# Performance work log

Hardware: AMD Instinct MI355X
Metric: run time of the kernel (lower is better)

Reference implementation:

```python
import jax, jax.numpy as jnp
import numpy as np


def setup_inputs() -> dict:
    key = jax.random.key(0)
    k1, k2 = jax.random.split(key)
    B, N, F, K = 8, 8192, 128, 512
    x = jax.random.normal(k1, (B, N, F), dtype=jnp.float32)
    cluster_centers = jax.random.normal(k2, (K, F), dtype=jnp.float32)
    return {"x": x, "cluster_centers": cluster_centers}


def reference(x, cluster_centers):
    # same math as sqrt(sum((x - c)^2)) without the [B,N,K,F] intermediate).
    x_sq = jnp.sum(x * x, axis=-1, keepdims=True)                 # [B, N, 1]
    c_sq = jnp.sum(cluster_centers * cluster_centers, axis=-1)    # [K]
    cross = jnp.einsum("bnf,kf->bnk", x, cluster_centers)         # [B, N, K]
    d2 = jnp.maximum(x_sq + c_sq[None, None, :] - 2.0 * cross, 0.0)
    distances = jnp.sqrt(d2)                                      # [B, N, K]
    associations = jax.nn.softmax(-distances, axis=-1)            # [B, N, K]
    output = jnp.einsum("bnk,kf->bnf", associations, cluster_centers)
    return output
```

## Files before the change

kernel.cpp:

```cpp
#include <hip/hip_runtime.h>
#include <hip/hip_bf16.h>

typedef short v8s __attribute__((ext_vector_type(8)));
typedef float v16f __attribute__((ext_vector_type(16)));
typedef unsigned v2u __attribute__((ext_vector_type(2)));

#define F_ 128
#define K_ 512
#define M_ 65536
#define CB_CH 9216
#define CT_CH 8192
#define CT_BASE 73728

typedef __attribute__((address_space(1))) const char gch;
typedef __attribute__((address_space(3))) char lch;

__device__ __forceinline__ short f2bf(float f) {
    union { float f; unsigned u; } v; v.f = f;
    unsigned u = v.u;
    u = (u + 0x7FFFu + ((u >> 16) & 1u)) >> 16;
    return (short)u;
}
__device__ __forceinline__ float bf2f(short s) {
    union { float f; unsigned u; } v;
    v.u = ((unsigned)(unsigned short)s) << 16;
    return v.f;
}

#if __has_builtin(__builtin_amdgcn_permlane32_swap)
#define HAVE_PLS 1
#endif

__device__ __forceinline__ void pswap(unsigned &a, unsigned &b, int lane) {
#ifdef HAVE_PLS
    v2u r = __builtin_amdgcn_permlane32_swap(a, b, false, false);
    a = (unsigned)r.x; b = (unsigned)r.y;
#else
    unsigned sa = (unsigned)__shfl_xor((int)a, 32);
    unsigned sb = (unsigned)__shfl_xor((int)b, 32);
    if (lane & 32) a = sb; else b = sa;
#endif
}

__global__ void prep_kernel(const float* __restrict__ centers, short* __restrict__ G) {
    const int c = blockIdx.x;
    const int f = threadIdx.x;
    const int ch = c >> 6, c64 = c & 63;
    float v = centers[c * F_ + f];
    short b = f2bf(v);
    float vb = bf2f(b);
    { const int ks = f >> 4, h = (f >> 3) & 1, j = f & 7;
      G[(size_t)ch * CB_CH + (size_t)((ks * 2 + h) * 64 + c64) * 8 + j] = b; }
    { const int kap = c64 >> 4, hh = (c64 >> 3) & 1, jj = c64 & 7;
      G[CT_BASE + (size_t)ch * CT_CH + (size_t)((kap * 2 + hh) * F_ + f) * 8 + jj] = b; }
    float s = vb * vb;
    #pragma unroll
    for (int off = 1; off < 64; off <<= 1) s += __shfl_xor(s, off);
    __shared__ float part[2];
    if ((f & 63) == 0) part[f >> 6] = s;
    __syncthreads();
    if (f < 16) {
        const float csq = part[0] + part[1];
        const float chv = -0.5f * csq;
        const short vh = f2bf(chv);
        const short vl = f2bf(chv - bf2f(vh));
        const short val = (f == 0) ? vh : (f == 1) ? vl : (f == 2) ? (short)0x3F80 : (short)0;
        const int h2 = f >> 3, j2 = f & 7;
        G[(size_t)ch * CB_CH + (size_t)((16 + h2) * 64 + c64) * 8 + j2] = val;
    }
}

__global__ __launch_bounds__(512, 2) void cluster_kernel(
        const float* __restrict__ x, const short* __restrict__ G,
        float* __restrict__ out) {
    __shared__ __align__(16) short SBall[CT_BASE];
    const int tid = threadIdx.x;
    const int wave = tid >> 6, lane = tid & 63;
    const int h = lane >> 5, c32 = lane & 31;
    const int row0 = blockIdx.x * 256 + wave * 32;

    {
        lch* d = (lch*)SBall;
        #pragma unroll
        for (int t = 0; t < 18; ++t) {
            const int gbase = t * 512 + wave * 64;
            __builtin_amdgcn_global_load_lds((gch*)((const char*)G + (size_t)(gbase + lane) * 16),
                                             d + (size_t)gbase * 16, 16, 0, 0);
        }
    }

    const float4* xr4 = (const float4*)(x + (size_t)(row0 + c32) * F_);
    float4 xl[16];
    #pragma unroll
    for (int ks = 0; ks < 8; ++ks) {
        xl[2 * ks]     = xr4[ks * 4 + h * 2];
        xl[2 * ks + 1] = xr4[ks * 4 + h * 2 + 1];
    }
    v8s Bx[9];
    float xs = 0.f;
    #pragma unroll
    for (int ks = 0; ks < 8; ++ks) {
        float vv[8] = {xl[2*ks].x, xl[2*ks].y, xl[2*ks].z, xl[2*ks].w,
                       xl[2*ks+1].x, xl[2*ks+1].y, xl[2*ks+1].z, xl[2*ks+1].w};
        v8s fr;
        #pragma unroll
        for (int j = 0; j < 8; ++j) {
            short bb = f2bf(vv[j]);
            fr[j] = bb;
            float r = bf2f(bb);
            xs += r * r;
        }
        Bx[ks] = fr;
    }
    xs += __shfl_xor(xs, 32);
    {
        const float xh = -0.5f * xs;
        const short sxh = f2bf(xh);
        const short sxl = f2bf(xh - bf2f(sxh));
        v8s e = (v8s){0, 0, 0, 0, 0, 0, 0, 0};
        if (h == 0) { e[0] = (short)0x3F80; e[1] = (short)0x3F80; e[2] = sxh; e[3] = sxl; }
        Bx[8] = e;
    }

    v16f Of[4];
    #pragma unroll
    for (int ft = 0; ft < 4; ++ft)
        #pragma unroll
        for (int e2 = 0; e2 < 16; ++e2) Of[ft][e2] = 0.f;
    float lden = 0.f;

    __syncthreads();

    #pragma unroll 1
    for (int j = 0; j < 8; ++j) {
        const int ch = (wave + blockIdx.x + j) & 7;
        const short* CbS = SBall + (size_t)ch * CB_CH;
        const short* CTGc = G + CT_BASE + (size_t)ch * CT_CH;

        v8s cf0[8];
        #pragma unroll
        for (int kp = 0; kp < 2; ++kp)
            #pragma unroll
            for (int ft = 0; ft < 4; ++ft)
                cf0[kp * 4 + ft] = *(const v8s*)
                    &CTGc[(size_t)((kp * 2 + h) * F_ + ft * 32 + c32) * 8];

        v16f a0, a1;
        #pragma unroll
        for (int e2 = 0; e2 < 16; ++e2) { a0[e2] = 0.f; a1[e2] = 0.f; }
        {
            v8s f0a = *(const v8s*)&CbS[(size_t)((0 * 2 + h) * 64 + c32) * 8];
            v8s f1a = *(const v8s*)&CbS[(size_t)((0 * 2 + h) * 64 + 32 + c32) * 8];
            v8s f0b = *(const v8s*)&CbS[(size_t)((1 * 2 + h) * 64 + c32) * 8];
            v8s f1b = *(const v8s*)&CbS[(size_t)((1 * 2 + h) * 64 + 32 + c32) * 8];
            #pragma unroll
            for (int ks = 0; ks < 9; ++ks) {
                v8s c0 = f0a, c1 = f1a;
                f0a = f0b; f1a = f1b;
                if (ks < 7) {
                    f0b = *(const v8s*)&CbS[(size_t)(((ks + 2) * 2 + h) * 64 + c32) * 8];
                    f1b = *(const v8s*)&CbS[(size_t)(((ks + 2) * 2 + h) * 64 + 32 + c32) * 8];
                }
                a0 = __builtin_amdgcn_mfma_f32_32x32x16_bf16(c0, Bx[ks], a0, 0, 0, 0);
                a1 = __builtin_amdgcn_mfma_f32_32x32x16_bf16(c1, Bx[ks], a1, 0, 0, 0);
            }
        }

        unsigned U[8];
        #pragma unroll
        for (int t = 0; t < 8; ++t) {
            const float s20 = fmaxf(-4.16273796f * a0[2 * t], 0.f);
            const float s21 = fmaxf(-4.16273796f * a0[2 * t + 1], 0.f);
            const float p0 = __builtin_amdgcn_exp2f(-__builtin_amdgcn_sqrtf(s20));
            const float p1 = __builtin_amdgcn_exp2f(-__builtin_amdgcn_sqrtf(s21));
            union { __hip_bfloat162 hh; unsigned u; } cv;
            cv.hh = __float22bfloat162_rn(make_float2(p0, p1));
            U[t] = cv.u;
            lden += __uint_as_float(cv.u << 16);
            lden += __uint_as_float(cv.u & 0xffff0000u);
        }
        v8s cf1[8];
        #pragma unroll
        for (int kp = 0; kp < 2; ++kp)
            #pragma unroll
            for (int ft = 0; ft < 4; ++ft)
                cf1[kp * 4 + ft] = *(const v8s*)
                    &CTGc[(size_t)(((2 + kp) * 2 + h) * F_ + ft * 32 + c32) * 8];
        #pragma unroll
        for (int kp = 0; kp < 2; ++kp) {
            unsigned s0 = U[4 * kp],     s2 = U[4 * kp + 2];
            unsigned s1 = U[4 * kp + 1], s3 = U[4 * kp + 3];
            pswap(s0, s2, lane);
            pswap(s1, s3, lane);
            union { v8s v; unsigned u[4]; } pf;
            pf.u[0] = s0; pf.u[1] = s1; pf.u[2] = s2; pf.u[3] = s3;
            #pragma unroll
            for (int ft = 0; ft < 4; ++ft)
                Of[ft] = __builtin_amdgcn_mfma_f32_32x32x16_bf16(pf.v, cf0[kp * 4 + ft], Of[ft], 0, 0, 0);
        }
        #pragma unroll
        for (int t = 0; t < 8; ++t) {
            const float s20 = fmaxf(-4.16273796f * a1[2 * t], 0.f);
            const float s21 = fmaxf(-4.16273796f * a1[2 * t + 1], 0.f);
            const float p0 = __builtin_amdgcn_exp2f(-__builtin_amdgcn_sqrtf(s20));
            const float p1 = __builtin_amdgcn_exp2f(-__builtin_amdgcn_sqrtf(s21));
            union { __hip_bfloat162 hh; unsigned u; } cv;
            cv.hh = __float22bfloat162_rn(make_float2(p0, p1));
            U[t] = cv.u;
            lden += __uint_as_float(cv.u << 16);
            lden += __uint_as_float(cv.u & 0xffff0000u);
        }
        #pragma unroll
        for (int kp = 0; kp < 2; ++kp) {
            unsigned s0 = U[4 * kp],     s2 = U[4 * kp + 2];
            unsigned s1 = U[4 * kp + 1], s3 = U[4 * kp + 3];
            pswap(s0, s2, lane);
            pswap(s1, s3, lane);
            union { v8s v; unsigned u[4]; } pf;
            pf.u[0] = s0; pf.u[1] = s1; pf.u[2] = s2; pf.u[3] = s3;
            #pragma unroll
            for (int ft = 0; ft < 4; ++ft)
                Of[ft] = __builtin_amdgcn_mfma_f32_32x32x16_bf16(pf.v, cf1[kp * 4 + ft], Of[ft], 0, 0, 0);
        }
    }

    lden += __shfl_xor(lden, 32);
    const float inv = 1.0f / lden;
    float invr[16];
    #pragma unroll
    for (int r = 0; r < 16; ++r)
        invr[r] = __shfl(inv, (r & 3) + 8 * (r >> 2) + 4 * h);
    #pragma unroll
    for (int ft = 0; ft < 4; ++ft)
        #pragma unroll
        for (int r = 0; r < 16; ++r) {
            const int xrow = (r & 3) + 8 * (r >> 2) + 4 * h;
            out[(size_t)(row0 + xrow) * F_ + ft * 32 + c32] = Of[ft][r] * invr[r];
        }
}

extern "C" void kernel_launch(void* const* d_in, const int* in_sizes, int n_in,
                              void* d_out, int out_size, void* d_ws, size_t ws_size,
                              hipStream_t stream) {
    const float* x       = (const float*)d_in[0];
    const float* centers = (const float*)d_in[1];
    float* out = (float*)d_out;
    short* G = (short*)d_ws;
    prep_kernel<<<K_, F_, 0, stream>>>(centers, G);
    cluster_kernel<<<M_ / 256, 512, 0, stream>>>(x, G, out);
}
```

Before: 106.1 us.

## Software-pipeline distance MFMAs one half-chunk ahead of softmax and output MFMAs

Restructures the 8-chunk loop into 15 half-chunk steps. Each step computes the next 32-center distance tile into a ping-pong accumulator while the current tile's exp/sqrt and output MFMAs run, and prefetches the next center-transpose fragments from global memory after use. The aim is to overlap the transcendental VALU work and global loads with MFMA work. In exchange it uses extra accumulator registers and a runtime-selected ping-pong that the compiler may turn into register moves, and it drops the old LDS double-buffered fragment prefetch.

Result: no change. 107.9 us (+1.7%).

```diff
diff --git a/kernel.cpp b/kernel.cpp
--- a/kernel.cpp
+++ b/kernel.cpp
@@ -78,6 +78,7 @@
     const int wave = tid >> 6, lane = tid & 63;
     const int h = lane >> 5, c32 = lane & 31;
     const int row0 = blockIdx.x * 256 + wave * 32;
+    const int wv_off = (wave + blockIdx.x) & 7;
 
     {
         lch* d = (lch*)SBall;
@@ -131,46 +132,52 @@
 
     __syncthreads();
 
+    v16f accA, accB;
+    v8s cf[8];
+
+    {
+        const short* CbS = SBall + (size_t)wv_off * CB_CH;
+        #pragma unroll
+        for (int e2 = 0; e2 < 16; ++e2) accA[e2] = 0.f;
+        #pragma unroll
+        for (int ks = 0; ks < 9; ++ks) {
+            v8s af = *(const v8s*)&CbS[(size_t)((ks * 2 + h) * 64 + c32) * 8];
+            accA = __builtin_amdgcn_mfma_f32_32x32x16_bf16(af, Bx[ks], accA, 0, 0, 0);
+        }
+        const short* CTGc = G + CT_BASE + (size_t)wv_off * CT_CH;
+        #pragma unroll
+        for (int kp = 0; kp < 2; ++kp)
+            #pragma unroll
+            for (int ft = 0; ft < 4; ++ft)
+                cf[kp * 4 + ft] = *(const v8s*)
+                    &CTGc[(size_t)((kp * 2 + h) * F_ + ft * 32 + c32) * 8];
+    }
+
     #pragma unroll 1
-    for (int j = 0; j < 8; ++j) {
-        const int ch = (wave + blockIdx.x + j) & 7;
-        const short* CbS = SBall + (size_t)ch * CB_CH;
-        const short* CTGc = G + CT_BASE + (size_t)ch * CT_CH;
-
-        v8s cf0[8];
-        #pragma unroll
-        for (int kp = 0; kp < 2; ++kp)
-            #pragma unroll
-            for (int ft = 0; ft < 4; ++ft)
-                cf0[kp * 4 + ft] = *(const v8s*)
-                    &CTGc[(size_t)((kp * 2 + h) * F_ + ft * 32 + c32) * 8];
-
-        v16f a0, a1;
-        #pragma unroll
-        for (int e2 = 0; e2 < 16; ++e2) { a0[e2] = 0.f; a1[e2] = 0.f; }
+    for (int tau = 0; tau < 15; ++tau) {
+        const int tn = tau + 1;
+        const int chn = (wv_off + (tn >> 1)) & 7, ctn = tn & 1;
+
         {
-            v8s f0a = *(const v8s*)&CbS[(size_t)((0 * 2 + h) * 64 + c32) * 8];
-            v8s f1a = *(const v8s*)&CbS[(size_t)((0 * 2 + h) * 64 + 32 + c32) * 8];
-            v8s f0b = *(const v8s*)&CbS[(size_t)((1 * 2 + h) * 64 + c32) * 8];
-            v8s f1b = *(const v8s*)&CbS[(size_t)((1 * 2 + h) * 64 + 32 + c32) * 8];
+            const short* CbS = SBall + (size_t)chn * CB_CH;
+            const int cb = ctn * 32 + c32;
+            v16f an;
+            #pragma unroll
+            for (int e2 = 0; e2 < 16; ++e2) an[e2] = 0.f;
             #pragma unroll
             for (int ks = 0; ks < 9; ++ks) {
-                v8s c0 = f0a, c1 = f1a;
-                f0a = f0b; f1a = f1b;
-                if (ks < 7) {
-                    f0b = *(const v8s*)&CbS[(size_t)(((ks + 2) * 2 + h) * 64 + c32) * 8];
-                    f1b = *(const v8s*)&CbS[(size_t)(((ks + 2) * 2 + h) * 64 + 32 + c32) * 8];
-                }
-                a0 = __builtin_amdgcn_mfma_f32_32x32x16_bf16(c0, Bx[ks], a0, 0, 0, 0);
-                a1 = __builtin_amdgcn_mfma_f32_32x32x16_bf16(c1, Bx[ks], a1, 0, 0, 0);
+                v8s af = *(const v8s*)&CbS[(size_t)((ks * 2 + h) * 64 + cb) * 8];
+                an = __builtin_amdgcn_mfma_f32_32x32x16_bf16(af, Bx[ks], an, 0, 0, 0);
             }
-        }
-
+            if (tau & 1) accA = an; else accB = an;
+        }
+
+        const v16f acc = (tau & 1) ? accB : accA;
         unsigned U[8];
         #pragma unroll
         for (int t = 0; t < 8; ++t) {
-            const float s20 = fmaxf(-4.16273796f * a0[2 * t], 0.f);
-            const float s21 = fmaxf(-4.16273796f * a0[2 * t + 1], 0.f);
+            const float s20 = fmaxf(-4.16273796f * acc[2 * t], 0.f);
+            const float s21 = fmaxf(-4.16273796f * acc[2 * t + 1], 0.f);
             const float p0 = __builtin_amdgcn_exp2f(-__builtin_amdgcn_sqrtf(s20));
             const float p1 = __builtin_amdgcn_exp2f(-__builtin_amdgcn_sqrtf(s21));
             union { __hip_bfloat162 hh; unsigned u; } cv;
@@ -179,13 +186,7 @@
             lden += __uint_as_float(cv.u << 16);
             lden += __uint_as_float(cv.u & 0xffff0000u);
         }
-        v8s cf1[8];
-        #pragma unroll
-        for (int kp = 0; kp < 2; ++kp)
-            #pragma unroll
-            for (int ft = 0; ft < 4; ++ft)
-                cf1[kp * 4 + ft] = *(const v8s*)
-                    &CTGc[(size_t)(((2 + kp) * 2 + h) * F_ + ft * 32 + c32) * 8];
+
         #pragma unroll
         for (int kp = 0; kp < 2; ++kp) {
             unsigned s0 = U[4 * kp],     s2 = U[4 * kp + 2];
@@ -196,12 +197,27 @@
             pf.u[0] = s0; pf.u[1] = s1; pf.u[2] = s2; pf.u[3] = s3;
             #pragma unroll
             for (int ft = 0; ft < 4; ++ft)
-                Of[ft] = __builtin_amdgcn_mfma_f32_32x32x16_bf16(pf.v, cf0[kp * 4 + ft], Of[ft], 0, 0, 0);
-        }
+                Of[ft] = __builtin_amdgcn_mfma_f32_32x32x16_bf16(pf.v, cf[kp * 4 + ft], Of[ft], 0, 0, 0);
+        }
+
+        {
+            const short* CTGc = G + CT_BASE + (size_t)chn * CT_CH;
+            #pragma unroll
+            for (int kp = 0; kp < 2; ++kp)
+                #pragma unroll
+                for (int ft = 0; ft < 4; ++ft)
+                    cf[kp * 4 + ft] = *(const v8s*)
+                        &CTGc[(size_t)(((ctn * 2 + kp) * 2 + h) * F_ + ft * 32 + c32) * 8];
+        }
+    }
+
+    {
+        const v16f acc = accB;
+        unsigned U[8];
         #pragma unroll
         for (int t = 0; t < 8; ++t) {
-            const float s20 = fmaxf(-4.16273796f * a1[2 * t], 0.f);
-            const float s21 = fmaxf(-4.16273796f * a1[2 * t + 1], 0.f);
+            const float s20 = fmaxf(-4.16273796f * acc[2 * t], 0.f);
+            const float s21 = fmaxf(-4.16273796f * acc[2 * t + 1], 0.f);
             const float p0 = __builtin_amdgcn_exp2f(-__builtin_amdgcn_sqrtf(s20));
             const float p1 = __builtin_amdgcn_exp2f(-__builtin_amdgcn_sqrtf(s21));
             union { __hip_bfloat162 hh; unsigned u; } cv;
@@ -220,7 +236,7 @@
             pf.u[0] = s0; pf.u[1] = s1; pf.u[2] = s2; pf.u[3] = s3;
             #pragma unroll
             for (int ft = 0; ft < 4; ++ft)
-                Of[ft] = __builtin_amdgcn_mfma_f32_32x32x16_bf16(pf.v, cf1[kp * 4 + ft], Of[ft], 0, 0, 0);
+                Of[ft] = __builtin_amdgcn_mfma_f32_32x32x16_bf16(pf.v, cf[kp * 4 + ft], Of[ft], 0, 0, 0);
         }
     }
 
```
